# Kernel tuning notes

Measured on AMD Instinct MI355X. Metric: run time of the kernel, lower is better.

## Reference

```python
import jax, jax.numpy as jnp
import numpy as np

B, S, E, HEADS = 2, 2048, 2048, 16


def setup_inputs() -> dict:
    key = jax.random.key(0)
    k1, k2, k3 = jax.random.split(key, 3)
    x = jax.random.normal(k1, (B, S, E), dtype=jnp.float32)
    # Linear weights stored as (in, out); torch uses y = x @ W.T with W (out, in) -- same math.
    W_qkvh = jax.random.normal(k2, (E, 3 * E + HEADS), dtype=jnp.float32) * (E ** -0.5)
    W_out = jax.random.normal(k3, (E, E), dtype=jnp.float32) * (E ** -0.5)
    return {"x": x, "W_qkvh": W_qkvh, "W_out": W_out}


def reference(x, W_qkvh, W_out):
    b, s, e = x.shape
    heads = W_qkvh.shape[1] - 3 * e
    d = e // heads
    scale = e ** 0.5

    proj = x @ W_qkvh                                  # (b, s, 3e + heads)
    QKV, Hg = proj[..., : 3 * e], proj[..., 3 * e:]
    Hg = jnp.tanh(Hg).transpose(0, 2, 1)[..., None]    # (b, h, s, 1) gate
    QKV = QKV.reshape(b, s, heads, 3 * d).transpose(0, 2, 1, 3)  # (b, h, s, 3d)
    Q, K, V = jnp.split(QKV, 3, axis=-1)               # each (b, h, s, d)

    # Cummean(H*K) along seq: cumsum(n * x) / n^2 with n = 1..s
    n = jnp.arange(1, s + 1, dtype=x.dtype).reshape(1, 1, s, 1)
    Kc = jnp.cumsum(n * (Hg * K), axis=2) / (n * n)    # (b, h, s, d)

    scores = jnp.einsum('bhqd,bhkd->bhqk', Q, Kc) / scale
    causal = jnp.triu(jnp.ones((s, s), dtype=bool), k=1)
    scores = jnp.where(causal, -jnp.inf, scores)
    attn = jax.nn.softmax(scores, axis=-1)

    out = jnp.einsum('bhqk,bhkd->bhqd', attn, V)       # (b, h, s, d)
    out = out.transpose(0, 2, 1, 3).reshape(b, s, e)
    return out @ W_out
```

## Files before the change

### kernel.cpp

```cpp
#include <hip/hip_runtime.h>
#include <hip/hip_bf16.h>
#include <math.h>

#define PB 2
#define PS 2048
#define PE 2048
#define PH 16
#define PD 128
#define PN_PROJ 6160
#define PM 4096

typedef __attribute__((ext_vector_type(8))) short bf16x8;
typedef __attribute__((ext_vector_type(4))) float f32x4;

__device__ __forceinline__ void gload_lds16(const void* g, void* l) {
  __builtin_amdgcn_global_load_lds((const __attribute__((address_space(1))) void*)g,
                                   (__attribute__((address_space(3))) void*)l, 16, 0, 0);
}

__global__ __launch_bounds__(512, 1) void gemm_qkv(
    const __hip_bfloat16* __restrict__ A, const __hip_bfloat16* __restrict__ Bt,
    __hip_bfloat16* __restrict__ Qp, __hip_bfloat16* __restrict__ Kp,
    __hip_bfloat16* __restrict__ Vtp, int K, int nTilesX) {
  constexpr int BM = 128, BN = 384, WM = 2, WN = 4;
  constexpr int MF = BM / WM / 16;
  constexpr int NF = BN / WN / 16;
  constexpr int SLOT = (BM + BN) * 64;
  constexpr int AL = BM / 64;
  constexpr int BL = BN / 64;
  constexpr int NLD = AL + BL;

  __shared__ __align__(16) __hip_bfloat16 lds[2 * SLOT];

  const int tid = threadIdx.x;
  const int w = tid >> 6, lane = tid & 63;
  const int fq = lane >> 4, fr = lane & 15;
  const int wm = w / WN, wn = w % WN;

  const int total = gridDim.x;
  const int swz = (blockIdx.x & 7) * (total >> 3) + (blockIdx.x >> 3);
  const int mBase = (swz / nTilesX) * BM;
  const int h = swz % nTilesX;
  const int nBase = h * BN;

  const int srow = tid >> 3, sc = tid & 7;

  auto stage = [&](int t) {
    char* base = (char*)lds + (size_t)(t & 1) * SLOT * 2;
#pragma unroll
    for (int l = 0; l < AL; ++l) {
      int row = l * 64 + srow;
      int cs = sc ^ (row & 7);
      gload_lds16(A + (size_t)(mBase + row) * K + t * 64 + cs * 8,
                  base + l * 8192 + w * 1024);
    }
#pragma unroll
    for (int l = 0; l < BL; ++l) {
      int row = l * 64 + srow;
      int cs = sc ^ (row & 7);
      gload_lds16(Bt + (size_t)(nBase + row) * K + t * 64 + cs * 8,
                  base + BM * 128 + l * 8192 + w * 1024);
    }
  };

  f32x4 acc[MF][NF];
#pragma unroll
  for (int m = 0; m < MF; ++m)
#pragma unroll
    for (int n = 0; n < NF; ++n) acc[m][n] = (f32x4){0.f, 0.f, 0.f, 0.f};

  const int NT = K / 64;
  stage(0); stage(1);

#pragma unroll 1
  for (int t = 0; t < NT; ++t) {
    if (t + 1 < NT) asm volatile("s_waitcnt vmcnt(%0)" ::"i"(NLD) : "memory");
    else            asm volatile("s_waitcnt vmcnt(0)" ::: "memory");
    __builtin_amdgcn_s_barrier();
    __builtin_amdgcn_sched_barrier(0);

    const __hip_bfloat16* sl = lds + (size_t)(t & 1) * SLOT;

    bf16x8 av[MF], bv[NF];
#pragma unroll
    for (int m = 0; m < MF; ++m) {
      int row = wm * (BM / WM) + m * 16 + fr;
      av[m] = *(const bf16x8*)&sl[row * 64 + ((fq ^ (row & 7)) * 8)];
    }
#pragma unroll
    for (int n = 0; n < NF; ++n) {
      int row = wn * (BN / WN) + n * 16 + fr;
      bv[n] = *(const bf16x8*)&sl[BM * 64 + row * 64 + ((fq ^ (row & 7)) * 8)];
    }
    asm volatile("s_waitcnt lgkmcnt(0)" ::: "memory");
    __builtin_amdgcn_sched_barrier(0);
    __builtin_amdgcn_s_setprio(1);
#pragma unroll
    for (int m = 0; m < MF; ++m)
#pragma unroll
      for (int n = 0; n < NF; ++n)
        acc[m][n] = __builtin_amdgcn_mfma_f32_16x16x32_bf16(av[m], bv[n], acc[m][n], 0, 0, 0);
    __builtin_amdgcn_s_setprio(0);

#pragma unroll
    for (int m = 0; m < MF; ++m) {
      int row = wm * (BM / WM) + m * 16 + fr;
      av[m] = *(const bf16x8*)&sl[row * 64 + (((4 + fq) ^ (row & 7)) * 8)];
    }
#pragma unroll
    for (int n = 0; n < NF; ++n) {
      int row = wn * (BN / WN) + n * 16 + fr;
      bv[n] = *(const bf16x8*)&sl[BM * 64 + row * 64 + (((4 + fq) ^ (row & 7)) * 8)];
    }
    asm volatile("s_waitcnt lgkmcnt(0)" ::: "memory");
    __builtin_amdgcn_s_barrier();
    __builtin_amdgcn_sched_barrier(0);
    if (t + 2 < NT) stage(t + 2);
    __builtin_amdgcn_s_setprio(1);
#pragma unroll
    for (int m = 0; m < MF; ++m)
#pragma unroll
      for (int n = 0; n < NF; ++n)
        acc[m][n] = __builtin_amdgcn_mfma_f32_16x16x32_bf16(av[m], bv[n], acc[m][n], 0, 0, 0);
    __builtin_amdgcn_s_setprio(0);
  }

#pragma unroll
  for (int m = 0; m < MF; ++m) {
#pragma unroll
    for (int n = 0; n < NF; ++n) {
      int row0 = mBase + wm * (BM / WM) + m * 16 + fq * 4;
      int colL = wn * (BN / WN) + n * 16 + fr;
      int which = colL >> 7;
      int d = colL & 127;
      int b = row0 >> 11, s0 = row0 & (PS - 1);
      if (which == 2) {
        union { __hip_bfloat16 hh[4]; uint2 u; } pk;
#pragma unroll
        for (int j = 0; j < 4; ++j) pk.hh[j] = __float2bfloat16(acc[m][n][j]);
        *(uint2*)&Vtp[(((size_t)(b * PH + h)) * PD + d) * PS + s0] = pk.u;
      } else {
        __hip_bfloat16* dst = which == 0 ? Qp : Kp;
#pragma unroll
        for (int j = 0; j < 4; ++j)
          dst[(((size_t)(b * PH + h)) * PS + s0 + j) * PD + d] = __float2bfloat16(acc[m][n][j]);
      }
    }
  }
}

template <int BM, int BN, int WM, int WN, typename OutT>
__global__ __launch_bounds__(512, 1) void gemm_cs3(
    const __hip_bfloat16* __restrict__ A, const __hip_bfloat16* __restrict__ Bt,
    OutT* __restrict__ C, int K, int lda, int ldb, int ldc, int nTilesX) {
  constexpr int MF = BM / WM / 16;
  constexpr int NF = BN / WN / 16;
  constexpr int SLOT = (BM + BN) * 64;
  constexpr int AL = BM / 64;
  constexpr int BL = BN / 64;
  constexpr int NLD = AL + BL;

  __shared__ __align__(16) __hip_bfloat16 lds[3 * SLOT];

  const int tid = threadIdx.x;
  const int w = tid >> 6, lane = tid & 63;
  const int fq = lane >> 4, fr = lane & 15;
  const int wm = w / WN, wn = w % WN;

  const int total = gridDim.x;
  const int swz = (blockIdx.x & 7) * (total >> 3) + (blockIdx.x >> 3);
  const int mBase = (swz / nTilesX) * BM;
  const int nBase = (swz % nTilesX) * BN;

  const int srow = tid >> 3, sc = tid & 7;

  auto stage = [&](int t) {
    char* base = (char*)lds + (size_t)(t % 3) * SLOT * 2;
#pragma unroll
    for (int l = 0; l < AL; ++l) {
      int row = l * 64 + srow;
      int cs = sc ^ (row & 7);
      gload_lds16(A + (size_t)(mBase + row) * lda + t * 64 + cs * 8,
                  base + l * 8192 + w * 1024);
    }
#pragma unroll
    for (int l = 0; l < BL; ++l) {
      int row = l * 64 + srow;
      int cs = sc ^ (row & 7);
      gload_lds16(Bt + (size_t)(nBase + row) * ldb + t * 64 + cs * 8,
                  base + BM * 128 + l * 8192 + w * 1024);
    }
  };

  f32x4 acc[MF][NF];
#pragma unroll
  for (int m = 0; m < MF; ++m)
#pragma unroll
    for (int n = 0; n < NF; ++n) acc[m][n] = (f32x4){0.f, 0.f, 0.f, 0.f};

  const int NT = K / 64;
  stage(0); stage(1);

#pragma unroll 1
  for (int t = 0; t < NT; ++t) {
    if (t + 1 < NT) asm volatile("s_waitcnt vmcnt(%0)" ::"i"(NLD) : "memory");
    else            asm volatile("s_waitcnt vmcnt(0)" ::: "memory");
    __builtin_amdgcn_s_barrier();
    __builtin_amdgcn_sched_barrier(0);
    if (t + 2 < NT) stage(t + 2);

    const __hip_bfloat16* sl = lds + (size_t)(t % 3) * SLOT;

#pragma unroll
    for (int kk = 0; kk < 2; ++kk) {
      bf16x8 av[MF], bv[NF];
#pragma unroll
      for (int m = 0; m < MF; ++m) {
        int row = wm * (BM / WM) + m * 16 + fr;
        av[m] = *(const bf16x8*)&sl[row * 64 + (((kk * 4 + fq) ^ (row & 7)) * 8)];
      }
#pragma unroll
      for (int n = 0; n < NF; ++n) {
        int row = wn * (BN / WN) + n * 16 + fr;
        bv[n] = *(const bf16x8*)&sl[BM * 64 + row * 64 + (((kk * 4 + fq) ^ (row & 7)) * 8)];
      }
      asm volatile("s_waitcnt lgkmcnt(0)" ::: "memory");
      __builtin_amdgcn_sched_barrier(0);
      __builtin_amdgcn_s_setprio(1);
#pragma unroll
      for (int m = 0; m < MF; ++m)
#pragma unroll
        for (int n = 0; n < NF; ++n)
          acc[m][n] = __builtin_amdgcn_mfma_f32_16x16x32_bf16(av[m], bv[n], acc[m][n], 0, 0, 0);
      __builtin_amdgcn_s_setprio(0);
    }
  }

#pragma unroll
  for (int m = 0; m < MF; ++m) {
#pragma unroll
    for (int n = 0; n < NF; ++n) {
      int row0 = mBase + wm * (BM / WM) + m * 16 + fq * 4;
      int col = nBase + wn * (BN / WN) + n * 16 + fr;
#pragma unroll
      for (int j = 0; j < 4; ++j) {
        if constexpr (__is_same(OutT, float))
          C[(size_t)(row0 + j) * ldc + col] = acc[m][n][j];
        else
          C[(size_t)(row0 + j) * ldc + col] = __float2bfloat16(acc[m][n][j]);
      }
    }
  }
}

__global__ __launch_bounds__(256) void transpose_cast(const float* __restrict__ W,
                                                      __hip_bfloat16* __restrict__ Wt,
                                                      int ldw, int ldt, int nOff) {
  __shared__ float t[32][33];
  int nb = blockIdx.x * 32, kb = blockIdx.y * 32;
  int tx = threadIdx.x & 31, ty = threadIdx.x >> 5;
#pragma unroll
  for (int i = 0; i < 4; ++i) {
    int k = ty + i * 8;
    t[k][tx] = W[(size_t)(kb + k) * ldw + nOff + nb + tx];
  }
  __syncthreads();
#pragma unroll
  for (int i = 0; i < 4; ++i) {
    int n = ty + i * 8;
    Wt[(size_t)(nb + n) * ldt + kb + tx] = __float2bfloat16(t[tx][n]);
  }
}

__global__ __launch_bounds__(256) void hg_from_x(const float* __restrict__ x,
                                                 const float* __restrict__ W,
                                                 float* __restrict__ hgbuf,
                                                 __hip_bfloat16* __restrict__ xb) {
  int bs = blockIdx.x;
  int b = bs >> 11, s = bs & (PS - 1);
  __shared__ float xs[PE];
  __shared__ float red[16][17];
  const float* xr = x + (size_t)bs * PE;
  for (int i = threadIdx.x; i < PE / 4; i += 256)
    *(float4*)&xs[i * 4] = ((const float4*)xr)[i];
  __syncthreads();
  {
    union { __hip_bfloat16 hh[8]; bf16x8 v; } pk;
#pragma unroll
    for (int k = 0; k < 8; ++k) pk.hh[k] = __float2bfloat16(xs[threadIdx.x * 8 + k]);
    *(bf16x8*)&xb[(size_t)bs * PE + threadIdx.x * 8] = pk.v;
  }
  int h = threadIdx.x & 15, part = threadIdx.x >> 4;
  float acc = 0.f;
  for (int k = part * 128; k < part * 128 + 128; ++k)
    acc += xs[k] * W[(size_t)k * PN_PROJ + 3 * PE + h];
  red[part][h] = acc;
  __syncthreads();
  if (threadIdx.x < 16) {
    float sm = 0.f;
#pragma unroll
    for (int p = 0; p < 16; ++p) sm += red[p][threadIdx.x];
    hgbuf[(size_t)(b * PH + threadIdx.x) * PS + s] = tanhf(sm);
  }
}

#define KC_SCALE 0.031879358f

__global__ __launch_bounds__(128) void kc_pass1(const __hip_bfloat16* __restrict__ Kp,
                                                const float* __restrict__ hgbuf,
                                                float* __restrict__ csum) {
  int c = blockIdx.x & 15, bh = blockIdx.x >> 4;
  int d = threadIdx.x;
  __shared__ float hgs[128];
  hgs[d] = hgbuf[(size_t)bh * PS + c * 128 + d];
  __syncthreads();
  const __hip_bfloat16* kb = Kp + ((size_t)bh * PS + c * 128) * PD + d;
  float acc = 0.f;
  int j0 = c * 128;
  for (int i = 0; i < 128; ++i)
    acc += (float)(j0 + i + 1) * hgs[i] * __bfloat162float(kb[(size_t)i * PD]);
  csum[blockIdx.x * 128 + d] = acc;
}

__global__ __launch_bounds__(128) void kc_pass2(__hip_bfloat16* __restrict__ Kp,
                                                const float* __restrict__ hgbuf,
                                                const float* __restrict__ csum) {
  int c = blockIdx.x & 15, bh = blockIdx.x >> 4;
  int d = threadIdx.x;
  __shared__ float hgs[128];
  hgs[d] = hgbuf[(size_t)bh * PS + c * 128 + d];
  __syncthreads();
  float acc = 0.f;
  for (int cc = 0; cc < c; ++cc) acc += csum[(bh * 16 + cc) * 128 + d];
  __hip_bfloat16* kb = Kp + ((size_t)bh * PS + c * 128) * PD + d;
  int j0 = c * 128;
  for (int i = 0; i < 128; ++i) {
    float t = (float)(j0 + i + 1);
    acc += t * hgs[i] * __bfloat162float(kb[(size_t)i * PD]);
    kb[(size_t)i * PD] = __float2bfloat16(acc / (t * t) * KC_SCALE);
  }
}

__global__ __launch_bounds__(256) void attn_mfma(const __hip_bfloat16* __restrict__ Qp,
                                                 const __hip_bfloat16* __restrict__ Kp,
                                                 const __hip_bfloat16* __restrict__ Vtp,
                                                 __hip_bfloat16* __restrict__ O) {
  const int qt = 15 - (blockIdx.x >> 5);
  const int bh = blockIdx.x & 31;
  const int b = bh >> 4, h = bh & 15;
  const int tid = threadIdx.x;
  const int w = tid >> 6, lane = tid & 63;
  const int fq = lane >> 4, fr = lane & 15;
  const int nt = (qt + 1) * 2;
  const int q0 = qt * 128;
  const int qw = q0 + w * 32;

  __shared__ __align__(16) char smem[58368];
  __hip_bfloat16* Psw = (__hip_bfloat16*)(smem + 49152) + w * 16 * 72;
  __hip_bfloat16* Os = (__hip_bfloat16*)(smem + 16384);

  const __hip_bfloat16* kb0 = Kp + (size_t)bh * PS * PD;
  const __hip_bfloat16* vb0 = Vtp + (size_t)bh * PD * PS;

  const int klr = lane >> 4, kc = lane & 15;
  const int vlr = lane >> 3, vc = lane & 7;

  auto stageK = [&](int t, int bufi) {
    char* ksb = smem + bufi * 16384;
    const __hip_bfloat16* kb = kb0 + (size_t)(t * 64) * PD;
#pragma unroll
    for (int p = 0; p < 4; ++p) {
      int row = w * 16 + p * 4 + klr;
      int cs = kc ^ (row & 7);
      gload_lds16(kb + (size_t)row * PD + cs * 8, ksb + (w * 16 + p * 4) * 256);
    }
  };
  auto stageV = [&](int t) {
    char* vsb = smem + 32768;
    const __hip_bfloat16* vb = vb0 + t * 64;
#pragma unroll
    for (int p = 0; p < 4; ++p) {
      int row = w * 32 + p * 8 + vlr;
      int cs = vc ^ (row & 7);
      gload_lds16(vb + (size_t)row * PS + cs * 8, vsb + (w * 32 + p * 8) * 128);
    }
  };

  const __hip_bfloat16* qbase = Qp + ((size_t)bh * PS + qw) * PD;
  bf16x8 qf[2][4];
#pragma unroll
  for (int r2 = 0; r2 < 2; ++r2)
#pragma unroll
    for (int kk = 0; kk < 4; ++kk)
      qf[r2][kk] = *(const bf16x8*)&qbase[(size_t)(r2 * 16 + fr) * PD + kk * 32 + fq * 8];

  stageK(0, 0);
  stageV(0);
  int cur = 0;

  f32x4 oacc[2][8];
#pragma unroll
  for (int r2 = 0; r2 < 2; ++r2)
#pragma unroll
    for (int nd = 0; nd < 8; ++nd) oacc[r2][nd] = (f32x4){0.f, 0.f, 0.f, 0.f};
  float m_[2] = {-__builtin_inff(), -__builtin_inff()};
  float l_[2] = {0.f, 0.f};

#pragma unroll 1
  for (int kt = 0; kt < nt; ++kt) {
    const bool hasNextK = (kt + 1 < nt);
    if (hasNextK) stageK(kt + 1, cur ^ 1);
    if (hasNextK) asm volatile("s_waitcnt vmcnt(8)" ::: "memory");
    else          asm volatile("s_waitcnt vmcnt(4)" ::: "memory");
    __builtin_amdgcn_s_barrier();
    __builtin_amdgcn_sched_barrier(0);

    const bool compute = (kt * 64 <= qw + 31);
    const bool diag = (kt * 64 + 63) > qw;
    const __hip_bfloat16* Ks = (const __hip_bfloat16*)(smem + cur * 16384);

    f32x4 sacc[2][4];
    if (compute) {
#pragma unroll
      for (int r2 = 0; r2 < 2; ++r2)
#pragma unroll
        for (int n = 0; n < 4; ++n) sacc[r2][n] = (f32x4){0.f, 0.f, 0.f, 0.f};
#pragma unroll
      for (int kk = 0; kk < 4; ++kk) {
#pragma unroll
        for (int n = 0; n < 4; ++n) {
          bf16x8 kf = *(const bf16x8*)&Ks[(n * 16 + fr) * 128 + (((kk * 4 + fq) ^ (fr & 7)) * 8)];
          sacc[0][n] = __builtin_amdgcn_mfma_f32_16x16x32_bf16(kf, qf[0][kk], sacc[0][n], 0, 0, 0);
          sacc[1][n] = __builtin_amdgcn_mfma_f32_16x16x32_bf16(kf, qf[1][kk], sacc[1][n], 0, 0, 0);
        }
      }
    }

    if (hasNextK) asm volatile("s_waitcnt vmcnt(4)" ::: "memory");
    else          asm volatile("s_waitcnt vmcnt(0)" ::: "memory");
    __builtin_amdgcn_s_barrier();
    __builtin_amdgcn_sched_barrier(0);

    if (compute) {
      const __hip_bfloat16* Vts = (const __hip_bfloat16*)(smem + 32768);
#pragma unroll
      for (int r2 = 0; r2 < 2; ++r2) {
        const int qg = qw + r2 * 16 + fr;
        float sv[4][4];
#pragma unroll
        for (int n = 0; n < 4; ++n)
#pragma unroll
          for (int j = 0; j < 4; ++j) sv[n][j] = sacc[r2][n][j];
        if (diag) {
#pragma unroll
          for (int n = 0; n < 4; ++n)
#pragma unroll
            for (int j = 0; j < 4; ++j)
              if ((kt * 64 + n * 16 + fq * 4 + j) > qg) sv[n][j] = -__builtin_inff();
        }
        float pmax = sv[0][0];
#pragma unroll
        for (int n = 0; n < 4; ++n)
#pragma unroll
          for (int j = 0; j < 4; ++j) pmax = fmaxf(pmax, sv[n][j]);
        pmax = fmaxf(pmax, __shfl_xor(pmax, 16, 64));
        pmax = fmaxf(pmax, __shfl_xor(pmax, 32, 64));

        const bool nof = __all(pmax <= m_[r2] + 11.5415605f);
        const float mn = nof ? m_[r2] : fmaxf(m_[r2], pmax);
        float ps = 0.f;
#pragma unroll
        for (int n = 0; n < 4; ++n) {
          union { __hip_bfloat16 hh[4]; uint2 u; } pkk;
#pragma unroll
          for (int j = 0; j < 4; ++j) {
            float p = exp2f(sv[n][j] - mn);
            ps += p;
            pkk.hh[j] = __float2bfloat16(p);
          }
          *(uint2*)&Psw[fr * 72 + n * 16 + fq * 4] = pkk.u;
        }
        ps += __shfl_xor(ps, 16, 64);
        ps += __shfl_xor(ps, 32, 64);

        if (!nof) {
          const float alpha = exp2f(m_[r2] - mn);
          l_[r2] = l_[r2] * alpha + ps;
          m_[r2] = mn;
          float a0 = __shfl(alpha, fq * 4 + 0, 64);
          float a1 = __shfl(alpha, fq * 4 + 1, 64);
          float a2 = __shfl(alpha, fq * 4 + 2, 64);
          float a3 = __shfl(alpha, fq * 4 + 3, 64);
#pragma unroll
          for (int nd = 0; nd < 8; ++nd) {
            oacc[r2][nd][0] *= a0; oacc[r2][nd][1] *= a1;
            oacc[r2][nd][2] *= a2; oacc[r2][nd][3] *= a3;
          }
        } else {
          l_[r2] += ps;
        }

#pragma unroll
        for (int kk2 = 0; kk2 < 2; ++kk2) {
          bf16x8 pa = *(const bf16x8*)&Psw[fr * 72 + kk2 * 32 + fq * 8];
#pragma unroll
          for (int nd = 0; nd < 8; ++nd) {
            bf16x8 vf = *(const bf16x8*)&Vts[(nd * 16 + fr) * 64 + (((kk2 * 4 + fq) ^ (fr & 7)) * 8)];
            oacc[r2][nd] = __builtin_amdgcn_mfma_f32_16x16x32_bf16(pa, vf, oacc[r2][nd], 0, 0, 0);
          }
        }
      }
    }

    asm volatile("s_waitcnt lgkmcnt(0)" ::: "memory");
    __builtin_amdgcn_sched_barrier(0);
    __builtin_amdgcn_s_barrier();
    if (kt + 1 < nt) stageV(kt + 1);
    cur ^= 1;
  }

  float i0 = 1.0f / l_[0], i1 = 1.0f / l_[1];
  float inv4[2][4];
#pragma unroll
  for (int j = 0; j < 4; ++j) {
    inv4[0][j] = __shfl(i0, fq * 4 + j, 64);
    inv4[1][j] = __shfl(i1, fq * 4 + j, 64);
  }
#pragma unroll
  for (int r2 = 0; r2 < 2; ++r2)
#pragma unroll
    for (int nd = 0; nd < 8; ++nd)
#pragma unroll
      for (int j = 0; j < 4; ++j)
        Os[(w * 32 + r2 * 16 + fq * 4 + j) * 136 + nd * 16 + fr] =
            __float2bfloat16(oacc[r2][nd][j] * inv4[r2][j]);
  __syncthreads();
#pragma unroll
  for (int it = 0; it < 8; ++it) {
    int i = it * 256 + tid;
    int row = i >> 4, ch = i & 15;
    *(bf16x8*)&O[(size_t)(b * PS + q0 + row) * PE + h * 128 + ch * 8] =
        *(const bf16x8*)&Os[row * 136 + ch * 8];
  }
}

extern "C" void kernel_launch(void* const* d_in, const int* in_sizes, int n_in,
                              void* d_out, int out_size, void* d_ws, size_t ws_size,
                              hipStream_t stream) {
  const float* x     = (const float*)d_in[0];
  const float* Wqkvh = (const float*)d_in[1];
  const float* Wout  = (const float*)d_in[2];
  float* out = (float*)d_out;

  const size_t HD = (size_t)PB * PH * PS * PD;
  char* wsb = (char*)d_ws;
  __hip_bfloat16* Qp = (__hip_bfloat16*)wsb;   wsb += HD * 2;
  __hip_bfloat16* Kp = (__hip_bfloat16*)wsb;   wsb += HD * 2;
  __hip_bfloat16* Vtp = (__hip_bfloat16*)wsb;  wsb += HD * 2;
  __hip_bfloat16* xb = (__hip_bfloat16*)wsb;   wsb += (size_t)PM * PE * 2;
  __hip_bfloat16* Wq_t = (__hip_bfloat16*)wsb; wsb += (size_t)3 * PE * PE * 2;
  __hip_bfloat16* Wout_t = (__hip_bfloat16*)wsb; wsb += (size_t)PE * PE * 2;
  float* hgbuf = (float*)wsb;                  wsb += (size_t)PB * PH * PS * 4;
  float* csum = (float*)wsb;

  hg_from_x<<<PM, 256, 0, stream>>>(x, Wqkvh, hgbuf, xb);
  transpose_cast<<<dim3(3 * PE / 32, PE / 32), 256, 0, stream>>>(Wqkvh, Wq_t, PN_PROJ, PE, 0);
  transpose_cast<<<dim3(PE / 32, PE / 32), 256, 0, stream>>>(Wout, Wout_t, PE, PE, 0);

  gemm_qkv<<<dim3((PM / 128) * PH), 512, 0, stream>>>(xb, Wq_t, Qp, Kp, Vtp, PE, PH);

  kc_pass1<<<PB * PH * 16, 128, 0, stream>>>(Kp, hgbuf, csum);
  kc_pass2<<<PB * PH * 16, 128, 0, stream>>>(Kp, hgbuf, csum);

  __hip_bfloat16* Ob = xb;
  attn_mfma<<<512, 256, 0, stream>>>(Qp, Kp, Vtp, Ob);

  gemm_cs3<128, 256, 2, 4, float>
      <<<dim3((PM / 128) * (PE / 256)), 512, 0, stream>>>(
          Ob, Wout_t, out, PE, PE, PE, PE, PE / 256);
}
```

Baseline: 322.1 us.

## Split attention block across eight waves with sixteen query rows each

The attention kernel now launches 512 threads per block, so each of eight waves handles 16 query rows instead of four waves handling 32. K/V staging is spread over all 512 threads and the wait counts are adjusted to the smaller number of outstanding loads. The aim is more waves per CU to hide latency and a lower per-wave register footprint, at the cost of each wave reading every K/V fragment for only one Q row tile, which halves LDS reuse per fragment and increases LDS traffic. LDS size grows to hold eight per-wave P buffers.

```diff
diff --git a/kernel.cpp b/kernel.cpp
--- a/kernel.cpp
+++ b/kernel.cpp
@@ -341,10 +341,10 @@
   }
 }
 
-__global__ __launch_bounds__(256) void attn_mfma(const __hip_bfloat16* __restrict__ Qp,
-                                                 const __hip_bfloat16* __restrict__ Kp,
-                                                 const __hip_bfloat16* __restrict__ Vtp,
-                                                 __hip_bfloat16* __restrict__ O) {
+__global__ __launch_bounds__(512, 1) void attn_mfma(const __hip_bfloat16* __restrict__ Qp,
+                                                    const __hip_bfloat16* __restrict__ Kp,
+                                                    const __hip_bfloat16* __restrict__ Vtp,
+                                                    __hip_bfloat16* __restrict__ O) {
   const int qt = 15 - (blockIdx.x >> 5);
   const int bh = blockIdx.x & 31;
   const int b = bh >> 4, h = bh & 15;
@@ -353,161 +353,151 @@
   const int fq = lane >> 4, fr = lane & 15;
   const int nt = (qt + 1) * 2;
   const int q0 = qt * 128;
-  const int qw = q0 + w * 32;
-
-  __shared__ __align__(16) char smem[58368];
+  const int qw = q0 + w * 16;
+
+  __shared__ __align__(16) char smem[67584];
   __hip_bfloat16* Psw = (__hip_bfloat16*)(smem + 49152) + w * 16 * 72;
   __hip_bfloat16* Os = (__hip_bfloat16*)(smem + 16384);
 
   const __hip_bfloat16* kb0 = Kp + (size_t)bh * PS * PD;
   const __hip_bfloat16* vb0 = Vtp + (size_t)bh * PD * PS;
-
-  const int klr = lane >> 4, kc = lane & 15;
-  const int vlr = lane >> 3, vc = lane & 7;
 
   auto stageK = [&](int t, int bufi) {
     char* ksb = smem + bufi * 16384;
     const __hip_bfloat16* kb = kb0 + (size_t)(t * 64) * PD;
 #pragma unroll
-    for (int p = 0; p < 4; ++p) {
-      int row = w * 16 + p * 4 + klr;
-      int cs = kc ^ (row & 7);
-      gload_lds16(kb + (size_t)row * PD + cs * 8, ksb + (w * 16 + p * 4) * 256);
+    for (int p = 0; p < 2; ++p) {
+      int s = p * 512 + tid;
+      int row = s >> 4, c = s & 15;
+      int cs = c ^ (row & 7);
+      gload_lds16(kb + (size_t)row * PD + cs * 8,
+                  ksb + (size_t)(p * 512 + (tid & ~63)) * 16);
     }
   };
   auto stageV = [&](int t) {
     char* vsb = smem + 32768;
     const __hip_bfloat16* vb = vb0 + t * 64;
 #pragma unroll
-    for (int p = 0; p < 4; ++p) {
-      int row = w * 32 + p * 8 + vlr;
-      int cs = vc ^ (row & 7);
-      gload_lds16(vb + (size_t)row * PS + cs * 8, vsb + (w * 32 + p * 8) * 128);
+    for (int p = 0; p < 2; ++p) {
+      int s = p * 512 + tid;
+      int row = s >> 3, c = s & 7;
+      int cs = c ^ (row & 7);
+      gload_lds16(vb + (size_t)row * PS + cs * 8,
+                  vsb + (size_t)(p * 512 + (tid & ~63)) * 16);
     }
   };
 
   const __hip_bfloat16* qbase = Qp + ((size_t)bh * PS + qw) * PD;
-  bf16x8 qf[2][4];
-#pragma unroll
-  for (int r2 = 0; r2 < 2; ++r2)
-#pragma unroll
-    for (int kk = 0; kk < 4; ++kk)
-      qf[r2][kk] = *(const bf16x8*)&qbase[(size_t)(r2 * 16 + fr) * PD + kk * 32 + fq * 8];
+  bf16x8 qf[4];
+#pragma unroll
+  for (int kk = 0; kk < 4; ++kk)
+    qf[kk] = *(const bf16x8*)&qbase[(size_t)fr * PD + kk * 32 + fq * 8];
 
   stageK(0, 0);
   stageV(0);
   int cur = 0;
 
-  f32x4 oacc[2][8];
-#pragma unroll
-  for (int r2 = 0; r2 < 2; ++r2)
-#pragma unroll
-    for (int nd = 0; nd < 8; ++nd) oacc[r2][nd] = (f32x4){0.f, 0.f, 0.f, 0.f};
-  float m_[2] = {-__builtin_inff(), -__builtin_inff()};
-  float l_[2] = {0.f, 0.f};
+  f32x4 oacc[8];
+#pragma unroll
+  for (int nd = 0; nd < 8; ++nd) oacc[nd] = (f32x4){0.f, 0.f, 0.f, 0.f};
+  float m_ = -__builtin_inff(), l_ = 0.f;
 
 #pragma unroll 1
   for (int kt = 0; kt < nt; ++kt) {
     const bool hasNextK = (kt + 1 < nt);
     if (hasNextK) stageK(kt + 1, cur ^ 1);
-    if (hasNextK) asm volatile("s_waitcnt vmcnt(8)" ::: "memory");
-    else          asm volatile("s_waitcnt vmcnt(4)" ::: "memory");
+    if (hasNextK) asm volatile("s_waitcnt vmcnt(4)" ::: "memory");
+    else          asm volatile("s_waitcnt vmcnt(2)" ::: "memory");
     __builtin_amdgcn_s_barrier();
     __builtin_amdgcn_sched_barrier(0);
 
-    const bool compute = (kt * 64 <= qw + 31);
+    const bool compute = (kt * 64 <= qw + 15);
     const bool diag = (kt * 64 + 63) > qw;
     const __hip_bfloat16* Ks = (const __hip_bfloat16*)(smem + cur * 16384);
 
-    f32x4 sacc[2][4];
+    f32x4 sacc[4];
     if (compute) {
 #pragma unroll
-      for (int r2 = 0; r2 < 2; ++r2)
-#pragma unroll
-        for (int n = 0; n < 4; ++n) sacc[r2][n] = (f32x4){0.f, 0.f, 0.f, 0.f};
+      for (int n = 0; n < 4; ++n) sacc[n] = (f32x4){0.f, 0.f, 0.f, 0.f};
 #pragma unroll
       for (int kk = 0; kk < 4; ++kk) {
 #pragma unroll
         for (int n = 0; n < 4; ++n) {
           bf16x8 kf = *(const bf16x8*)&Ks[(n * 16 + fr) * 128 + (((kk * 4 + fq) ^ (fr & 7)) * 8)];
-          sacc[0][n] = __builtin_amdgcn_mfma_f32_16x16x32_bf16(kf, qf[0][kk], sacc[0][n], 0, 0, 0);
-          sacc[1][n] = __builtin_amdgcn_mfma_f32_16x16x32_bf16(kf, qf[1][kk], sacc[1][n], 0, 0, 0);
+          sacc[n] = __builtin_amdgcn_mfma_f32_16x16x32_bf16(kf, qf[kk], sacc[n], 0, 0, 0);
         }
       }
     }
 
-    if (hasNextK) asm volatile("s_waitcnt vmcnt(4)" ::: "memory");
+    if (hasNextK) asm volatile("s_waitcnt vmcnt(2)" ::: "memory");
     else          asm volatile("s_waitcnt vmcnt(0)" ::: "memory");
     __builtin_amdgcn_s_barrier();
     __builtin_amdgcn_sched_barrier(0);
 
     if (compute) {
       const __hip_bfloat16* Vts = (const __hip_bfloat16*)(smem + 32768);
-#pragma unroll
-      for (int r2 = 0; r2 < 2; ++r2) {
-        const int qg = qw + r2 * 16 + fr;
-        float sv[4][4];
+      const int qg = qw + fr;
+      float sv[4][4];
+#pragma unroll
+      for (int n = 0; n < 4; ++n)
+#pragma unroll
+        for (int j = 0; j < 4; ++j) sv[n][j] = sacc[n][j];
+      if (diag) {
 #pragma unroll
         for (int n = 0; n < 4; ++n)
 #pragma unroll
-          for (int j = 0; j < 4; ++j) sv[n][j] = sacc[r2][n][j];
-        if (diag) {
-#pragma unroll
-          for (int n = 0; n < 4; ++n)
-#pragma unroll
-            for (int j = 0; j < 4; ++j)
-              if ((kt * 64 + n * 16 + fq * 4 + j) > qg) sv[n][j] = -__builtin_inff();
+          for (int j = 0; j < 4; ++j)
+            if ((kt * 64 + n * 16 + fq * 4 + j) > qg) sv[n][j] = -__builtin_inff();
+      }
+      float pmax = sv[0][0];
+#pragma unroll
+      for (int n = 0; n < 4; ++n)
+#pragma unroll
+        for (int j = 0; j < 4; ++j) pmax = fmaxf(pmax, sv[n][j]);
+      pmax = fmaxf(pmax, __shfl_xor(pmax, 16, 64));
+      pmax = fmaxf(pmax, __shfl_xor(pmax, 32, 64));
+
+      const bool nof = __all(pmax <= m_ + 11.5415605f);
+      const float mn = nof ? m_ : fmaxf(m_, pmax);
+      float ps = 0.f;
+#pragma unroll
+      for (int n = 0; n < 4; ++n) {
+        union { __hip_bfloat16 hh[4]; uint2 u; } pkk;
+#pragma unroll
+        for (int j = 0; j < 4; ++j) {
+          float p = exp2f(sv[n][j] - mn);
+          ps += p;
+          pkk.hh[j] = __float2bfloat16(p);
         }
-        float pmax = sv[0][0];
-#pragma unroll
-        for (int n = 0; n < 4; ++n)
-#pragma unroll
-          for (int j = 0; j < 4; ++j) pmax = fmaxf(pmax, sv[n][j]);
-        pmax = fmaxf(pmax, __shfl_xor(pmax, 16, 64));
-        pmax = fmaxf(pmax, __shfl_xor(pmax, 32, 64));
-
-        const bool nof = __all(pmax <= m_[r2] + 11.5415605f);
-        const float mn = nof ? m_[r2] : fmaxf(m_[r2], pmax);
-        float ps = 0.f;
-#pragma unroll
-        for (int n = 0; n < 4; ++n) {
-          union { __hip_bfloat16 hh[4]; uint2 u; } pkk;
-#pragma unroll
-          for (int j = 0; j < 4; ++j) {
-            float p = exp2f(sv[n][j] - mn);
-            ps += p;
-            pkk.hh[j] = __float2bfloat16(p);
-          }
-          *(uint2*)&Psw[fr * 72 + n * 16 + fq * 4] = pkk.u;
+        *(uint2*)&Psw[fr * 72 + n * 16 + fq * 4] = pkk.u;
+      }
+      ps += __shfl_xor(ps, 16, 64);
+      ps += __shfl_xor(ps, 32, 64);
+
+      if (!nof) {
+        const float alpha = exp2f(m_ - mn);
+        l_ = l_ * alpha + ps;
+        m_ = mn;
+        float a0 = __shfl(alpha, fq * 4 + 0, 64);
+        float a1 = __shfl(alpha, fq * 4 + 1, 64);
+        float a2 = __shfl(alpha, fq * 4 + 2, 64);
+        float a3 = __shfl(alpha, fq * 4 + 3, 64);
+#pragma unroll
+        for (int nd = 0; nd < 8; ++nd) {
+          oacc[nd][0] *= a0; oacc[nd][1] *= a1;
+          oacc[nd][2] *= a2; oacc[nd][3] *= a3;
         }
-        ps += __shfl_xor(ps, 16, 64);
-        ps += __shfl_xor(ps, 32, 64);
-
-        if (!nof) {
-          const float alpha = exp2f(m_[r2] - mn);
-          l_[r2] = l_[r2] * alpha + ps;
-          m_[r2] = mn;
-          float a0 = __shfl(alpha, fq * 4 + 0, 64);
-          float a1 = __shfl(alpha, fq * 4 + 1, 64);
-          float a2 = __shfl(alpha, fq * 4 + 2, 64);
-          float a3 = __shfl(alpha, fq * 4 + 3, 64);
-#pragma unroll
-          for (int nd = 0; nd < 8; ++nd) {
-            oacc[r2][nd][0] *= a0; oacc[r2][nd][1] *= a1;
-            oacc[r2][nd][2] *= a2; oacc[r2][nd][3] *= a3;
-          }
-        } else {
-          l_[r2] += ps;
-        }
-
-#pragma unroll
-        for (int kk2 = 0; kk2 < 2; ++kk2) {
-          bf16x8 pa = *(const bf16x8*)&Psw[fr * 72 + kk2 * 32 + fq * 8];
-#pragma unroll
-          for (int nd = 0; nd < 8; ++nd) {
-            bf16x8 vf = *(const bf16x8*)&Vts[(nd * 16 + fr) * 64 + (((kk2 * 4 + fq) ^ (fr & 7)) * 8)];
-            oacc[r2][nd] = __builtin_amdgcn_mfma_f32_16x16x32_bf16(pa, vf, oacc[r2][nd], 0, 0, 0);
-          }
+      } else {
+        l_ += ps;
+      }
+
+#pragma unroll
+      for (int kk2 = 0; kk2 < 2; ++kk2) {
+        bf16x8 pa = *(const bf16x8*)&Psw[fr * 72 + kk2 * 32 + fq * 8];
+#pragma unroll
+        for (int nd = 0; nd < 8; ++nd) {
+          bf16x8 vf = *(const bf16x8*)&Vts[(nd * 16 + fr) * 64 + (((kk2 * 4 + fq) ^ (fr & 7)) * 8)];
+          oacc[nd] = __builtin_amdgcn_mfma_f32_16x16x32_bf16(pa, vf, oacc[nd], 0, 0, 0);
         }
       }
     }
@@ -519,25 +509,20 @@
     cur ^= 1;
   }
 
-  float i0 = 1.0f / l_[0], i1 = 1.0f / l_[1];
-  float inv4[2][4];
-#pragma unroll
-  for (int j = 0; j < 4; ++j) {
-    inv4[0][j] = __shfl(i0, fq * 4 + j, 64);
-    inv4[1][j] = __shfl(i1, fq * 4 + j, 64);
-  }
-#pragma unroll
-  for (int r2 = 0; r2 < 2; ++r2)
-#pragma unroll
-    for (int nd = 0; nd < 8; ++nd)
-#pragma unroll
-      for (int j = 0; j < 4; ++j)
-        Os[(w * 32 + r2 * 16 + fq * 4 + j) * 136 + nd * 16 + fr] =
-            __float2bfloat16(oacc[r2][nd][j] * inv4[r2][j]);
+  float inv = 1.0f / l_;
+  float inv4[4];
+#pragma unroll
+  for (int j = 0; j < 4; ++j) inv4[j] = __shfl(inv, fq * 4 + j, 64);
+#pragma unroll
+  for (int nd = 0; nd < 8; ++nd)
+#pragma unroll
+    for (int j = 0; j < 4; ++j)
+      Os[(w * 16 + fq * 4 + j) * 136 + nd * 16 + fr] =
+          __float2bfloat16(oacc[nd][j] * inv4[j]);
   __syncthreads();
 #pragma unroll
-  for (int it = 0; it < 8; ++it) {
-    int i = it * 256 + tid;
+  for (int it = 0; it < 4; ++it) {
+    int i = it * 512 + tid;
     int row = i >> 4, ch = i & 15;
     *(bf16x8*)&O[(size_t)(b * PS + q0 + row) * PE + h * 128 + ch * 8] =
         *(const bf16x8*)&Os[row * 136 + ch * 8];
@@ -573,7 +558,7 @@
   kc_pass2<<<PB * PH * 16, 128, 0, stream>>>(Kp, hgbuf, csum);
 
   __hip_bfloat16* Ob = xb;
-  attn_mfma<<<512, 256, 0, stream>>>(Qp, Kp, Vtp, Ob);
+  attn_mfma<<<512, 512, 0, stream>>>(Qp, Kp, Vtp, Ob);
 
   gemm_cs3<128, 256, 2, 4, float>
       <<<dim3((PM / 128) * (PE / 256)), 512, 0, stream>>>(
```

New measurement: 294.1 us. -8.7%, faster.
